# Kernel tuning notes

Measured on AMD Instinct MI355X. Metric: run time of the kernel, lower is better.

## Reference

```python
import jax, jax.numpy as jnp
import numpy as np

B, S, D_IN, D_FF, D_OUT, E = 4, 2048, 1024, 4096, 1024, 8


def setup_inputs() -> dict:
    key = jax.random.key(0)
    ks = jax.random.split(key, 8)
    s = lambda k, shape, fan: jax.random.normal(k, shape, dtype=jnp.float32) * (1.0 / np.sqrt(fan))
    return {
        "x": jax.random.normal(ks[0], (B, S, D_IN), dtype=jnp.float32),
        "switch_w": s(ks[1], (D_IN, E), D_IN),
        "switch_b": jnp.zeros((E,), dtype=jnp.float32),
        "w1": s(ks[2], (E, D_IN, D_FF), D_IN),
        "b1": jnp.zeros((E, D_FF), dtype=jnp.float32),
        "w2": s(ks[3], (E, D_FF, D_OUT), D_FF),
        "b2": jnp.zeros((E, D_OUT), dtype=jnp.float32),
    }


def reference(x, switch_w, switch_b, w1, b1, w2, b2):
    b, s, d = x.shape
    n_experts = w1.shape[0]
    xf = x.reshape(-1, d)                                   # [T, d]
    route_prob = jax.nn.softmax(xf @ switch_w + switch_b, axis=-1)  # [T, E]
    route_prob_max = jnp.max(route_prob, axis=-1)           # [T]
    routes = jnp.argmax(route_prob, axis=-1)                # [T] int, constant wrt grads

    # Per-expert FFN applied to all tokens, combined with top-1 one-hot mask
    # (drop_tokens=False -> every token goes to exactly its argmax expert).
    h = jax.nn.relu(jnp.einsum('td,edf->etf', xf, w1) + b1[:, None, :])   # [E, T, f]
    y_all = jnp.einsum('etf,efo->eto', h, w2) + b2[:, None, :]            # [E, T, d_out]
    onehot = jax.nn.one_hot(routes, n_experts, dtype=xf.dtype)            # [T, E]
    y = jnp.einsum('eto,te->to', y_all, onehot)             # dispatch-combine

    # is_scale_prob=True: scale output by routing probability
    y = y * route_prob_max[:, None]

    counts = onehot.sum(axis=0)                             # tokens per expert
    route_frac = counts / counts.sum()
    aux_loss = n_experts * jnp.sum(route_frac * route_prob.sum(axis=0))

    return y.reshape(b, s, -1), aux_loss
```

## Files before the change

kernel.cpp:

```cpp
#include <hip/hip_runtime.h>
#include <cstdint>
#include <cstddef>

#define NT   8192
#define DIN  1024
#define DFF  4096
#define DOUT 1024
#define NEXP 8

typedef float  f32x4v __attribute__((ext_vector_type(4)));
typedef short  s16x8  __attribute__((ext_vector_type(8)));
typedef short  s16x4  __attribute__((ext_vector_type(4)));

__device__ __forceinline__ ushort f2bf(float f) {
  union { float f; uint32_t u; } c; c.f = f;
  uint32_t u = c.u;
  return (ushort)((u + 0x7fffu + ((u >> 16) & 1u)) >> 16);
}

__global__ __launch_bounds__(256) void router_kernel(
    const float* __restrict__ x, const float* __restrict__ sw,
    const float* __restrict__ sb,
    int* __restrict__ routes, int* __restrict__ posArr,
    float* __restrict__ pmaxArr,
    int* __restrict__ cnt, float* __restrict__ probsum) {
  __shared__ int   sRoute[64];
  __shared__ float sProb[4][NEXP];
  __shared__ int   sBase[NEXP];

  const int lane = threadIdx.x & 63;
  const int w    = threadIdx.x >> 6;
  const int t0   = blockIdx.x * 64;

  float bias[NEXP];
#pragma unroll
  for (int e = 0; e < NEXP; e++) bias[e] = sb[e];

  float wprob[NEXP];
#pragma unroll
  for (int e = 0; e < NEXP; e++) wprob[e] = 0.0f;

  for (int k = 0; k < 16; k++) {
    const int t = t0 + w * 16 + k;
    const float* xr = x + (size_t)t * DIN;
    float acc[NEXP];
#pragma unroll
    for (int e = 0; e < NEXP; e++) acc[e] = 0.0f;
#pragma unroll
    for (int it = 0; it < DIN / 64; it++) {
      const int i = it * 64 + lane;
      const float xv = xr[i];
      const float4 s0 = *(const float4*)(sw + (size_t)i * NEXP);
      const float4 s1 = *(const float4*)(sw + (size_t)i * NEXP + 4);
      acc[0] += xv * s0.x; acc[1] += xv * s0.y; acc[2] += xv * s0.z; acc[3] += xv * s0.w;
      acc[4] += xv * s1.x; acc[5] += xv * s1.y; acc[6] += xv * s1.z; acc[7] += xv * s1.w;
    }
#pragma unroll
    for (int e = 0; e < NEXP; e++) {
#pragma unroll
      for (int off = 32; off > 0; off >>= 1) acc[e] += __shfl_xor(acc[e], off, 64);
    }
    float m = acc[0] + bias[0]; int am = 0;
    float lg[NEXP];
#pragma unroll
    for (int e = 0; e < NEXP; e++) {
      lg[e] = acc[e] + bias[e];
      if (lg[e] > m) { m = lg[e]; am = e; }
    }
    float esum = 0.0f;
    float pe[NEXP];
#pragma unroll
    for (int e = 0; e < NEXP; e++) { pe[e] = __expf(lg[e] - m); esum += pe[e]; }
    const float inv = 1.0f / esum;
#pragma unroll
    for (int e = 0; e < NEXP; e++) wprob[e] += pe[e] * inv;
    if (lane == 0) {
      routes[t] = am;
      pmaxArr[t] = inv;
      sRoute[w * 16 + k] = am;
    }
  }
  if (lane == 0) {
#pragma unroll
    for (int e = 0; e < NEXP; e++) sProb[w][e] = wprob[e];
  }
  __syncthreads();

  const int tid = threadIdx.x;
  if (tid < NEXP) {
    float s = sProb[0][tid] + sProb[1][tid] + sProb[2][tid] + sProb[3][tid];
    atomicAdd(&probsum[tid], s);
    int c = 0;
#pragma unroll
    for (int j = 0; j < 64; j++) c += (sRoute[j] == tid);
    sBase[tid] = atomicAdd(&cnt[tid], c);
  }
  __syncthreads();

  if (tid < 64) {
    const int r = sRoute[tid];
    int rank = 0;
    for (int j = 0; j < 64; j++) rank += (j < tid) & (sRoute[j] == r);
    posArr[t0 + tid] = sBase[r] + rank;
  }
}

__global__ void offsets_aux_kernel(const int* __restrict__ cnt, const float* __restrict__ probsum,
                                   int* __restrict__ offsets, float* __restrict__ auxout) {
  if (threadIdx.x == 0) {
    int o = 0; float aux = 0.0f;
    for (int e = 0; e < NEXP; e++) {
      offsets[e] = o; o += cnt[e];
      aux += (float)cnt[e] * probsum[e];
    }
    offsets[NEXP] = o;
    auxout[0] = aux * ((float)NEXP / (float)NT);
  }
}

__global__ void gather_kernel(const float* __restrict__ x, const int* __restrict__ routes,
                              const int* __restrict__ posArr, const int* __restrict__ offsets,
                              int* __restrict__ perm, ushort* __restrict__ Xg) {
  const int lane = threadIdx.x & 63;
  const int t = (blockIdx.x * blockDim.x + threadIdx.x) >> 6;
  if (t >= NT) return;
  const int slot = offsets[routes[t]] + posArr[t];
  if (lane == 0) perm[slot] = t;
  const float* src = x + (size_t)t * DIN;
  ushort* dst = Xg + (size_t)slot * DIN;
#pragma unroll
  for (int half = 0; half < 2; half++) {
    int i = half * 512 + lane * 8;
    float4 v0 = *(const float4*)(src + i);
    float4 v1 = *(const float4*)(src + i + 4);
    s16x8 p;
    p[0] = (short)f2bf(v0.x); p[1] = (short)f2bf(v0.y);
    p[2] = (short)f2bf(v0.z); p[3] = (short)f2bf(v0.w);
    p[4] = (short)f2bf(v1.x); p[5] = (short)f2bf(v1.y);
    p[6] = (short)f2bf(v1.z); p[7] = (short)f2bf(v1.w);
    *(s16x8*)(dst + i) = p;
  }
}

__global__ void transpose_cvt_kernel(const float* __restrict__ src, ushort* __restrict__ dst,
                                     const int K, const int N) {
  __shared__ float tile[64][65];
  const int ntn = N >> 6;
  const int ntk = K >> 6;
  int b = blockIdx.x;
  const int tn = b % ntn; b /= ntn;
  const int tk = b % ntk; const int e = b / ntk;
  const float* s = src + ((size_t)e * K + (size_t)tk * 64) * N + (size_t)tn * 64;
  const int c4 = (threadIdx.x & 15) * 4;
  const int r0 = threadIdx.x >> 4;
#pragma unroll
  for (int p = 0; p < 4; p++) {
    const int row = r0 + p * 16;
    float4 v = *(const float4*)(s + (size_t)row * N + c4);
    tile[row][c4 + 0] = v.x; tile[row][c4 + 1] = v.y;
    tile[row][c4 + 2] = v.z; tile[row][c4 + 3] = v.w;
  }
  __syncthreads();
  ushort* d = dst + ((size_t)e * N + (size_t)tn * 64) * K + (size_t)tk * 64;
#pragma unroll
  for (int p = 0; p < 4; p++) {
    const int nrow = r0 + p * 16;
    s16x4 o;
    o[0] = (short)f2bf(tile[c4 + 0][nrow]);
    o[1] = (short)f2bf(tile[c4 + 1][nrow]);
    o[2] = (short)f2bf(tile[c4 + 2][nrow]);
    o[3] = (short)f2bf(tile[c4 + 3][nrow]);
    *(s16x4*)(d + (size_t)nrow * K + c4) = o;
  }
}

#define GLD16(g, l)                                                                        \
  __builtin_amdgcn_global_load_lds((const __attribute__((address_space(1))) uint32_t*)(g), \
                                   (__attribute__((address_space(3))) uint32_t*)(l), 16, 0, 0)

#define SBAR()   asm volatile("s_barrier" ::: "memory")
#define WAITV(n) asm volatile("s_waitcnt vmcnt(" #n ")" ::: "memory")

template <int KDIM, int EPI>
__global__ __launch_bounds__(512, 1) void moe_gemm256_kernel(
    const ushort* __restrict__ A,
    const ushort* __restrict__ BT,
    const float* __restrict__ bias,
    const int* __restrict__ offsets,
    ushort* __restrict__ Hout,
    float* __restrict__ Y,
    const int* __restrict__ perm, const float* __restrict__ pmaxArr,
    const int N) {
  __shared__ ushort sA[4][8192];
  __shared__ ushort sB[4][8192];
  const int e = blockIdx.z;
  const int mlimit = offsets[e + 1];
  const int m0 = offsets[e] + blockIdx.y * 256;
  if (m0 >= mlimit) return;
  const int n0 = blockIdx.x * 256;
  const int tid = threadIdx.x;
  const int lane = tid & 63;
  const int wid = tid >> 6;
  const int wr = wid >> 2;
  const int wc = wid & 3;
  const int rsel = lane & 15;
  const int lhi = lane >> 4;

  const int srow = wid * 8 + (lane >> 3);
  const int scol = ((lane & 7) ^ (lane >> 3)) * 8;
  const ushort* gA = A + (size_t)(m0 + srow) * KDIM + scol;
  const ushort* gB = BT + ((size_t)e * N + n0 + srow) * KDIM + scol;
  const int ldst = tid * 8;

#define STAGE_A(s, h, kt)                                                   \
  do {                                                                      \
    const ushort* g_ = gA + (size_t)((h) * 128) * KDIM + (size_t)(kt) * 64; \
    GLD16(g_, &sA[s][ldst]);                                                \
    GLD16(g_ + (size_t)64 * KDIM, &sA[s][ldst + 4096]);                     \
  } while (0)
#define STAGE_B(s, h, kt)                                                   \
  do {                                                                      \
    const ushort* g_ = gB + (size_t)((h) * 128) * KDIM + (size_t)(kt) * 64; \
    GLD16(g_, &sB[s][ldst]);                                                \
    GLD16(g_ + (size_t)64 * KDIM, &sB[s][ldst + 4096]);                     \
  } while (0)

  f32x4v acc[2][2][4][2];
#pragma unroll
  for (int i = 0; i < 2; i++)
#pragma unroll
    for (int j = 0; j < 2; j++)
#pragma unroll
      for (int mf = 0; mf < 4; mf++)
#pragma unroll
        for (int nf = 0; nf < 2; nf++) acc[i][j][mf][nf] = (f32x4v)0.0f;

  const int rsw = rsel & 7;
  const int sw0 = ((lhi) ^ rsw) * 8;
  const int sw1 = ((4 + lhi) ^ rsw) * 8;
  int arow[4], brow[2];
#pragma unroll
  for (int mf = 0; mf < 4; mf++) arow[mf] = (wr * 64 + mf * 16 + rsel) * 64;
#pragma unroll
  for (int nf = 0; nf < 2; nf++) brow[nf] = (wc * 32 + nf * 16 + rsel) * 64;

  s16x8 a[4][2], b0[2][2], b1[2][2];

#define LDA(slot)                                                      \
  do {                                                                 \
    _Pragma("unroll") for (int mf = 0; mf < 4; mf++) {                 \
      a[mf][0] = *(const s16x8*)&sA[slot][arow[mf] + sw0];             \
      a[mf][1] = *(const s16x8*)&sA[slot][arow[mf] + sw1];             \
    }                                                                  \
  } while (0)
#define LDB(dst, slot)                                                 \
  do {                                                                 \
    _Pragma("unroll") for (int nf = 0; nf < 2; nf++) {                 \
      dst[nf][0] = *(const s16x8*)&sB[slot][brow[nf] + sw0];           \
      dst[nf][1] = *(const s16x8*)&sB[slot][brow[nf] + sw1];           \
    }                                                                  \
  } while (0)
#define MFMAQ(MG, NG, BB)                                              \
  do {                                                                 \
    __builtin_amdgcn_s_setprio(1);                                     \
    _Pragma("unroll") for (int mf = 0; mf < 4; mf++)                   \
    _Pragma("unroll") for (int nf = 0; nf < 2; nf++)                   \
    _Pragma("unroll") for (int ks = 0; ks < 2; ks++)                   \
      acc[MG][NG][mf][nf] = __builtin_amdgcn_mfma_f32_16x16x32_bf16(   \
          a[mf][ks], BB[nf][ks], acc[MG][NG][mf][nf], 0, 0, 0);        \
    __builtin_amdgcn_s_setprio(0);                                     \
  } while (0)

  constexpr int NS = KDIM / 64;
  STAGE_A(0, 0, 0);
  STAGE_B(0, 0, 0);
  STAGE_B(1, 1, 0);
  STAGE_A(1, 1, 0);
  WAITV(4);
  SBAR();

#pragma unroll 2
  for (int t = 0; t < NS; ++t) {
    const int s0 = (2 * t) & 3, s1 = (2 * t + 1) & 3;
    const int sn0 = (2 * t + 2) & 3, sn1 = (2 * t + 3) & 3;
    const bool more = (t + 1 < NS);
    LDA(s0);
    LDB(b0, s0);
    if (more) { STAGE_A(sn0, 0, t + 1); STAGE_B(sn0, 0, t + 1); }
    SBAR();
    MFMAQ(0, 0, b0);
    if (more) { WAITV(4); } else { WAITV(0); }
    SBAR();
    LDB(b1, s1);
    if (more) STAGE_B(sn1, 1, t + 1);
    SBAR();
    MFMAQ(0, 1, b1);
    SBAR();
    LDA(s1);
    if (more) STAGE_A(sn1, 1, t + 1);
    SBAR();
    MFMAQ(1, 1, b1);
    SBAR();
    MFMAQ(1, 0, b0);
    if (more) { WAITV(4); }
    SBAR();
  }
#undef LDA
#undef LDB
#undef MFMAQ
#undef STAGE_A
#undef STAGE_B

  float bv[2][2];
#pragma unroll
  for (int ng = 0; ng < 2; ng++)
#pragma unroll
    for (int nf = 0; nf < 2; nf++)
      bv[ng][nf] = bias[(size_t)e * N + n0 + ng * 128 + wc * 32 + nf * 16 + rsel];
#pragma unroll
  for (int mg = 0; mg < 2; mg++) {
#pragma unroll
    for (int mf = 0; mf < 4; mf++) {
#pragma unroll
      for (int r = 0; r < 4; r++) {
        const int grow = m0 + mg * 128 + wr * 64 + mf * 16 + lhi * 4 + r;
        if (grow < mlimit) {
          if (EPI == 0) {
            ushort* hrow = Hout + (size_t)grow * N + n0;
#pragma unroll
            for (int ng = 0; ng < 2; ng++)
#pragma unroll
              for (int nf = 0; nf < 2; nf++) {
                float v = acc[mg][ng][mf][nf][r] + bv[ng][nf];
                hrow[ng * 128 + wc * 32 + nf * 16 + rsel] = f2bf(fmaxf(v, 0.0f));
              }
          } else {
            const int tok = perm[grow];
            const float sc = pmaxArr[tok];
            float* yrow = Y + (size_t)tok * N + n0;
#pragma unroll
            for (int ng = 0; ng < 2; ng++)
#pragma unroll
              for (int nf = 0; nf < 2; nf++)
                yrow[ng * 128 + wc * 32 + nf * 16 + rsel] =
                    (acc[mg][ng][mf][nf][r] + bv[ng][nf]) * sc;
          }
        }
      }
    }
  }
}

extern "C" void kernel_launch(void* const* d_in, const int* in_sizes, int n_in,
                              void* d_out, int out_size, void* d_ws, size_t ws_size,
                              hipStream_t stream) {
  const float* x  = (const float*)d_in[0];
  const float* sw = (const float*)d_in[1];
  const float* sb = (const float*)d_in[2];
  const float* w1 = (const float*)d_in[3];
  const float* b1 = (const float*)d_in[4];
  const float* w2 = (const float*)d_in[5];
  const float* b2 = (const float*)d_in[6];
  float* out = (float*)d_out;
  float* auxp = out + (size_t)NT * DOUT;

  char* wsb = (char*)d_ws;
  int*   cnt      = (int*)wsb;
  float* probsum  = (float*)(wsb + 32);
  int*   offsets  = (int*)(wsb + 64);
  int*   routes   = (int*)(wsb + 256);
  int*   posArr   = routes + NT;
  float* pmaxArr  = (float*)(posArr + NT);
  int*   perm     = (int*)(pmaxArr + NT);
  ushort* Xg = (ushort*)(wsb + 256 + (size_t)4 * 4 * NT);
  ushort* Hg = Xg + (size_t)(NT + 256) * DIN;
  ushort* Wt = Hg + (size_t)(NT + 256) * DFF;
  size_t needed = (size_t)((char*)Wt - wsb) + (size_t)NEXP * DFF * DIN * 2;
  if (ws_size < needed) return;

  hipMemsetAsync(d_ws, 0, 64, stream);

  router_kernel<<<NT / 64, 256, 0, stream>>>(x, sw, sb, routes, posArr, pmaxArr, cnt, probsum);
  offsets_aux_kernel<<<1, 64, 0, stream>>>(cnt, probsum, offsets, auxp);
  gather_kernel<<<NT / 4, 256, 0, stream>>>(x, routes, posArr, offsets, perm, Xg);

  transpose_cvt_kernel<<<NEXP * (DIN / 64) * (DFF / 64), 256, 0, stream>>>(w1, Wt, DIN, DFF);
  moe_gemm256_kernel<DIN, 0><<<dim3(DFF / 256, 8, NEXP), 512, 0, stream>>>(
      Xg, Wt, b1, offsets, Hg, nullptr, nullptr, nullptr, DFF);

  transpose_cvt_kernel<<<NEXP * (DFF / 64) * (DOUT / 64), 256, 0, stream>>>(w2, Wt, DFF, DOUT);
  moe_gemm256_kernel<DFF, 1><<<dim3(DOUT / 256, 8, NEXP), 512, 0, stream>>>(
      Hg, Wt, b2, offsets, nullptr, out, perm, pmaxArr, DOUT);
}
```

Measured before the change: 356.7 us.

## Split-K the second expert GEMM and remap first GEMM grid for XCD locality

The down-projection GEMM is split into two K halves, doubling the number of blocks. The first half writes scaled output directly, the second writes bf16 partials that a new combine kernel adds into the output. The first GEMM uses a 1D grid remapped so each expert's tiles are grouped together, likely to improve L2 locality across XCDs. The split costs an extra partial write and read-modify-write pass, and the bf16 rounding of partials reduces accuracy.

```diff
diff --git a/kernel.cpp b/kernel.cpp
--- a/kernel.cpp
+++ b/kernel.cpp
@@ -16,6 +16,9 @@
   union { float f; uint32_t u; } c; c.f = f;
   uint32_t u = c.u;
   return (ushort)((u + 0x7fffu + ((u >> 16) & 1u)) >> 16);
+}
+__device__ __forceinline__ float bf2f(ushort h) {
+  union { uint32_t u; float f; } c; c.u = ((uint32_t)h) << 16; return c.f;
 }
 
 __global__ __launch_bounds__(256) void router_kernel(
@@ -189,15 +192,27 @@
     const int* __restrict__ offsets,
     ushort* __restrict__ Hout,
     float* __restrict__ Y,
+    ushort* __restrict__ P1,
     const int* __restrict__ perm, const float* __restrict__ pmaxArr,
-    const int N) {
+    const int N, const int LDK) {
   __shared__ ushort sA[4][8192];
   __shared__ ushort sB[4][8192];
-  const int e = blockIdx.z;
+  int e, bx, by, part;
+  if constexpr (EPI == 0) {
+    const int logical = ((blockIdx.x & 7) << 7) + (blockIdx.x >> 3);
+    e = logical >> 7;
+    bx = (logical & 127) >> 3;
+    by = logical & 7;
+    part = 0;
+  } else {
+    bx = blockIdx.x; by = blockIdx.y;
+    e = blockIdx.z & 7; part = blockIdx.z >> 3;
+  }
+  const size_t kofs = (size_t)part * KDIM;
   const int mlimit = offsets[e + 1];
-  const int m0 = offsets[e] + blockIdx.y * 256;
+  const int m0 = offsets[e] + by * 256;
   if (m0 >= mlimit) return;
-  const int n0 = blockIdx.x * 256;
+  const int n0 = bx * 256;
   const int tid = threadIdx.x;
   const int lane = tid & 63;
   const int wid = tid >> 6;
@@ -208,21 +223,21 @@
 
   const int srow = wid * 8 + (lane >> 3);
   const int scol = ((lane & 7) ^ (lane >> 3)) * 8;
-  const ushort* gA = A + (size_t)(m0 + srow) * KDIM + scol;
-  const ushort* gB = BT + ((size_t)e * N + n0 + srow) * KDIM + scol;
+  const ushort* gA = A + (size_t)(m0 + srow) * LDK + kofs + scol;
+  const ushort* gB = BT + ((size_t)e * N + n0 + srow) * LDK + kofs + scol;
   const int ldst = tid * 8;
 
-#define STAGE_A(s, h, kt)                                                   \
-  do {                                                                      \
-    const ushort* g_ = gA + (size_t)((h) * 128) * KDIM + (size_t)(kt) * 64; \
-    GLD16(g_, &sA[s][ldst]);                                                \
-    GLD16(g_ + (size_t)64 * KDIM, &sA[s][ldst + 4096]);                     \
+#define STAGE_A(s, h, kt)                                                  \
+  do {                                                                     \
+    const ushort* g_ = gA + (size_t)((h) * 128) * LDK + (size_t)(kt) * 64; \
+    GLD16(g_, &sA[s][ldst]);                                               \
+    GLD16(g_ + (size_t)64 * LDK, &sA[s][ldst + 4096]);                     \
   } while (0)
-#define STAGE_B(s, h, kt)                                                   \
-  do {                                                                      \
-    const ushort* g_ = gB + (size_t)((h) * 128) * KDIM + (size_t)(kt) * 64; \
-    GLD16(g_, &sB[s][ldst]);                                                \
-    GLD16(g_ + (size_t)64 * KDIM, &sB[s][ldst + 4096]);                     \
+#define STAGE_B(s, h, kt)                                                  \
+  do {                                                                     \
+    const ushort* g_ = gB + (size_t)((h) * 128) * LDK + (size_t)(kt) * 64; \
+    GLD16(g_, &sB[s][ldst]);                                               \
+    GLD16(g_ + (size_t)64 * LDK, &sB[s][ldst + 4096]);                     \
   } while (0)
 
   f32x4v acc[2][2][4][2];
@@ -325,7 +340,7 @@
       for (int r = 0; r < 4; r++) {
         const int grow = m0 + mg * 128 + wr * 64 + mf * 16 + lhi * 4 + r;
         if (grow < mlimit) {
-          if (EPI == 0) {
+          if constexpr (EPI == 0) {
             ushort* hrow = Hout + (size_t)grow * N + n0;
 #pragma unroll
             for (int ng = 0; ng < 2; ng++)
@@ -335,19 +350,54 @@
                 hrow[ng * 128 + wc * 32 + nf * 16 + rsel] = f2bf(fmaxf(v, 0.0f));
               }
           } else {
-            const int tok = perm[grow];
-            const float sc = pmaxArr[tok];
-            float* yrow = Y + (size_t)tok * N + n0;
-#pragma unroll
-            for (int ng = 0; ng < 2; ng++)
-#pragma unroll
-              for (int nf = 0; nf < 2; nf++)
-                yrow[ng * 128 + wc * 32 + nf * 16 + rsel] =
-                    (acc[mg][ng][mf][nf][r] + bv[ng][nf]) * sc;
+            if (part == 0) {
+              const int tok = perm[grow];
+              const float sc = pmaxArr[tok];
+              float* yrow = Y + (size_t)tok * N + n0;
+#pragma unroll
+              for (int ng = 0; ng < 2; ng++)
+#pragma unroll
+                for (int nf = 0; nf < 2; nf++)
+                  yrow[ng * 128 + wc * 32 + nf * 16 + rsel] =
+                      (acc[mg][ng][mf][nf][r] + bv[ng][nf]) * sc;
+            } else {
+              ushort* prow = P1 + (size_t)grow * N + n0;
+#pragma unroll
+              for (int ng = 0; ng < 2; ng++)
+#pragma unroll
+                for (int nf = 0; nf < 2; nf++)
+                  prow[ng * 128 + wc * 32 + nf * 16 + rsel] =
+                      f2bf(acc[mg][ng][mf][nf][r]);
+            }
           }
         }
       }
     }
+  }
+}
+
+__global__ __launch_bounds__(256) void combine_kernel(
+    const ushort* __restrict__ P1, const int* __restrict__ perm,
+    const float* __restrict__ pmaxArr, float* __restrict__ out) {
+  const int lane = threadIdx.x & 63;
+  const int slot = (blockIdx.x * blockDim.x + threadIdx.x) >> 6;
+  if (slot >= NT) return;
+  const int tok = perm[slot];
+  const float sc = pmaxArr[tok];
+  const ushort* src = P1 + (size_t)slot * DOUT;
+  float* dst = out + (size_t)tok * DOUT;
+#pragma unroll
+  for (int half = 0; half < 2; half++) {
+    const int i = half * 512 + lane * 8;
+    const s16x8 p = *(const s16x8*)(src + i);
+    float4 o0 = *(const float4*)(dst + i);
+    float4 o1 = *(const float4*)(dst + i + 4);
+    o0.x += sc * bf2f((ushort)p[0]); o0.y += sc * bf2f((ushort)p[1]);
+    o0.z += sc * bf2f((ushort)p[2]); o0.w += sc * bf2f((ushort)p[3]);
+    o1.x += sc * bf2f((ushort)p[4]); o1.y += sc * bf2f((ushort)p[5]);
+    o1.z += sc * bf2f((ushort)p[6]); o1.w += sc * bf2f((ushort)p[7]);
+    *(float4*)(dst + i) = o0;
+    *(float4*)(dst + i + 4) = o1;
   }
 }
 
@@ -377,6 +427,7 @@
   ushort* Wt = Hg + (size_t)(NT + 256) * DFF;
   size_t needed = (size_t)((char*)Wt - wsb) + (size_t)NEXP * DFF * DIN * 2;
   if (ws_size < needed) return;
+  ushort* P1 = Xg;
 
   hipMemsetAsync(d_ws, 0, 64, stream);
 
@@ -385,10 +436,11 @@
   gather_kernel<<<NT / 4, 256, 0, stream>>>(x, routes, posArr, offsets, perm, Xg);
 
   transpose_cvt_kernel<<<NEXP * (DIN / 64) * (DFF / 64), 256, 0, stream>>>(w1, Wt, DIN, DFF);
-  moe_gemm256_kernel<DIN, 0><<<dim3(DFF / 256, 8, NEXP), 512, 0, stream>>>(
-      Xg, Wt, b1, offsets, Hg, nullptr, nullptr, nullptr, DFF);
+  moe_gemm256_kernel<DIN, 0><<<1024, 512, 0, stream>>>(
+      Xg, Wt, b1, offsets, Hg, nullptr, nullptr, nullptr, nullptr, DFF, DIN);
 
   transpose_cvt_kernel<<<NEXP * (DFF / 64) * (DOUT / 64), 256, 0, stream>>>(w2, Wt, DFF, DOUT);
-  moe_gemm256_kernel<DFF, 1><<<dim3(DOUT / 256, 8, NEXP), 512, 0, stream>>>(
-      Hg, Wt, b2, offsets, nullptr, out, perm, pmaxArr, DOUT);
-}
+  moe_gemm256_kernel<DFF / 2, 3><<<dim3(DOUT / 256, 10, 16), 512, 0, stream>>>(
+      Hg, Wt, b2, offsets, nullptr, out, P1, perm, pmaxArr, DOUT, DFF);
+  combine_kernel<<<NT / 4, 256, 0, stream>>>(P1, perm, pmaxArr, out);
+}
```

Measured after the change: 393.8 us. 1.1x slower.

## Restructure MoE GEMM into 8-phase pipeline with two-tile-ahead prefetch and XCD-aware remap

Applied to the files above, without the earlier changes.

The GEMM main loop now prefetches two K-steps ahead, filling all four LDS slots up front, and waits on vmcnt(8) instead of keeping one step in flight. Each wave now covers a 128x64 output sub-tile, reading its A half and B half from slots picked by wave row and column, so LDS reads and MFMA phases are reorganised. The first GEMM also moves to a 1D grid with a remap that places each expert's tiles on a single XCD for L2 locality. The aim is better overlap of global loads with MFMA work and better cache reuse, at the cost of more loads in flight and a more complex slot scheme that is easy to get wrong.

```diff
diff --git a/kernel.cpp b/kernel.cpp
--- a/kernel.cpp
+++ b/kernel.cpp
@@ -182,7 +182,7 @@
 #define WAITV(n) asm volatile("s_waitcnt vmcnt(" #n ")" ::: "memory")
 
 template <int KDIM, int EPI>
-__global__ __launch_bounds__(512, 1) void moe_gemm256_kernel(
+__global__ __launch_bounds__(512, 1) void moe_gemm8p_kernel(
     const ushort* __restrict__ A,
     const ushort* __restrict__ BT,
     const float* __restrict__ bias,
@@ -191,18 +191,27 @@
     float* __restrict__ Y,
     const int* __restrict__ perm, const float* __restrict__ pmaxArr,
     const int N) {
-  __shared__ ushort sA[4][8192];
-  __shared__ ushort sB[4][8192];
-  const int e = blockIdx.z;
+  __shared__ ushort sA4[4][8192];
+  __shared__ ushort sB4[4][8192];
+  int e, bx, by;
+  if constexpr (EPI == 0) {
+    const int logical = ((blockIdx.x & 7) << 7) + (blockIdx.x >> 3);
+    e = logical >> 7;
+    bx = (logical & 127) >> 3;
+    by = logical & 7;
+  } else {
+    bx = blockIdx.x; by = blockIdx.y; e = blockIdx.z;
+  }
   const int mlimit = offsets[e + 1];
-  const int m0 = offsets[e] + blockIdx.y * 256;
+  const int m0 = offsets[e] + by * 256;
   if (m0 >= mlimit) return;
-  const int n0 = blockIdx.x * 256;
+  const int n0 = bx * 256;
   const int tid = threadIdx.x;
   const int lane = tid & 63;
   const int wid = tid >> 6;
   const int wr = wid >> 2;
   const int wc = wid & 3;
+  const int hb = wc >> 1;
   const int rsel = lane & 15;
   const int lhi = lane >> 4;
 
@@ -211,139 +220,134 @@
   const ushort* gA = A + (size_t)(m0 + srow) * KDIM + scol;
   const ushort* gB = BT + ((size_t)e * N + n0 + srow) * KDIM + scol;
   const int ldst = tid * 8;
-
-#define STAGE_A(s, h, kt)                                                   \
-  do {                                                                      \
-    const ushort* g_ = gA + (size_t)((h) * 128) * KDIM + (size_t)(kt) * 64; \
-    GLD16(g_, &sA[s][ldst]);                                                \
-    GLD16(g_ + (size_t)64 * KDIM, &sA[s][ldst + 4096]);                     \
-  } while (0)
-#define STAGE_B(s, h, kt)                                                   \
-  do {                                                                      \
-    const ushort* g_ = gB + (size_t)((h) * 128) * KDIM + (size_t)(kt) * 64; \
-    GLD16(g_, &sB[s][ldst]);                                                \
-    GLD16(g_ + (size_t)64 * KDIM, &sB[s][ldst + 4096]);                     \
-  } while (0)
-
-  f32x4v acc[2][2][4][2];
-#pragma unroll
-  for (int i = 0; i < 2; i++)
-#pragma unroll
-    for (int j = 0; j < 2; j++)
-#pragma unroll
-      for (int mf = 0; mf < 4; mf++)
-#pragma unroll
-        for (int nf = 0; nf < 2; nf++) acc[i][j][mf][nf] = (f32x4v)0.0f;
+  const size_t LK = (size_t)KDIM;
+
+#define STAGE_A(s, h, kt)                                              \
+  do {                                                                 \
+    const ushort* g_ = gA + (size_t)((h) * 128) * LK + (size_t)(kt) * 64; \
+    GLD16(g_, &sA4[s][ldst]);                                          \
+    GLD16(g_ + 64 * LK, &sA4[s][ldst + 4096]);                         \
+  } while (0)
+#define STAGE_B(s, h, kt)                                              \
+  do {                                                                 \
+    const ushort* g_ = gB + (size_t)((h) * 128) * LK + (size_t)(kt) * 64; \
+    GLD16(g_, &sB4[s][ldst]);                                          \
+    GLD16(g_ + 64 * LK, &sB4[s][ldst + 4096]);                         \
+  } while (0)
+
+  f32x4v acc[2][4][4];
+#pragma unroll
+  for (int g = 0; g < 2; g++)
+#pragma unroll
+    for (int mf = 0; mf < 4; mf++)
+#pragma unroll
+      for (int nf = 0; nf < 4; nf++) acc[g][mf][nf] = (f32x4v)0.0f;
 
   const int rsw = rsel & 7;
   const int sw0 = ((lhi) ^ rsw) * 8;
   const int sw1 = ((4 + lhi) ^ rsw) * 8;
-  int arow[4], brow[2];
-#pragma unroll
-  for (int mf = 0; mf < 4; mf++) arow[mf] = (wr * 64 + mf * 16 + rsel) * 64;
-#pragma unroll
-  for (int nf = 0; nf < 2; nf++) brow[nf] = (wc * 32 + nf * 16 + rsel) * 64;
+  const int arow0 = rsel * 64;
+  const int brow0 = ((wc & 1) * 64 + rsel) * 64;
 
   s16x8 a[4][2], b0[2][2], b1[2][2];
 
-#define LDA(slot)                                                      \
+#define LDA03(slot)                                                    \
   do {                                                                 \
     _Pragma("unroll") for (int mf = 0; mf < 4; mf++) {                 \
-      a[mf][0] = *(const s16x8*)&sA[slot][arow[mf] + sw0];             \
-      a[mf][1] = *(const s16x8*)&sA[slot][arow[mf] + sw1];             \
+      a[mf][0] = *(const s16x8*)&sA4[slot][arow0 + mf * 1024 + sw0];   \
+      a[mf][1] = *(const s16x8*)&sA4[slot][arow0 + mf * 1024 + sw1];   \
     }                                                                  \
   } while (0)
-#define LDB(dst, slot)                                                 \
+#define LDA47(slot)                                                    \
+  do {                                                                 \
+    _Pragma("unroll") for (int mf = 0; mf < 4; mf++) {                 \
+      a[mf][0] = *(const s16x8*)&sA4[slot][arow0 + 4096 + mf * 1024 + sw0]; \
+      a[mf][1] = *(const s16x8*)&sA4[slot][arow0 + 4096 + mf * 1024 + sw1]; \
+    }                                                                  \
+  } while (0)
+#define LDB2(dst, slot, nfb)                                           \
   do {                                                                 \
     _Pragma("unroll") for (int nf = 0; nf < 2; nf++) {                 \
-      dst[nf][0] = *(const s16x8*)&sB[slot][brow[nf] + sw0];           \
-      dst[nf][1] = *(const s16x8*)&sB[slot][brow[nf] + sw1];           \
+      dst[nf][0] = *(const s16x8*)&sB4[slot][brow0 + ((nfb) + nf) * 1024 + sw0]; \
+      dst[nf][1] = *(const s16x8*)&sB4[slot][brow0 + ((nfb) + nf) * 1024 + sw1]; \
     }                                                                  \
   } while (0)
-#define MFMAQ(MG, NG, BB)                                              \
+#define MFMAPH(MG, BB, NFB)                                            \
   do {                                                                 \
     __builtin_amdgcn_s_setprio(1);                                     \
     _Pragma("unroll") for (int mf = 0; mf < 4; mf++)                   \
     _Pragma("unroll") for (int nf = 0; nf < 2; nf++)                   \
     _Pragma("unroll") for (int ks = 0; ks < 2; ks++)                   \
-      acc[MG][NG][mf][nf] = __builtin_amdgcn_mfma_f32_16x16x32_bf16(   \
-          a[mf][ks], BB[nf][ks], acc[MG][NG][mf][nf], 0, 0, 0);        \
+      acc[MG][mf][(NFB) + nf] = __builtin_amdgcn_mfma_f32_16x16x32_bf16( \
+          a[mf][ks], BB[nf][ks], acc[MG][mf][(NFB) + nf], 0, 0, 0);    \
     __builtin_amdgcn_s_setprio(0);                                     \
   } while (0)
 
   constexpr int NS = KDIM / 64;
-  STAGE_A(0, 0, 0);
-  STAGE_B(0, 0, 0);
-  STAGE_B(1, 1, 0);
-  STAGE_A(1, 1, 0);
-  WAITV(4);
+  STAGE_A(0, 0, 0); STAGE_A(1, 1, 0); STAGE_B(0, 0, 0); STAGE_B(1, 1, 0);
+  STAGE_B(2, 0, 1); STAGE_B(3, 1, 1); STAGE_A(2, 0, 1); STAGE_A(3, 1, 1);
+  WAITV(8);
   SBAR();
 
 #pragma unroll 2
   for (int t = 0; t < NS; ++t) {
-    const int s0 = (2 * t) & 3, s1 = (2 * t + 1) & 3;
-    const int sn0 = (2 * t + 2) & 3, sn1 = (2 * t + 3) & 3;
-    const bool more = (t + 1 < NS);
-    LDA(s0);
-    LDB(b0, s0);
-    if (more) { STAGE_A(sn0, 0, t + 1); STAGE_B(sn0, 0, t + 1); }
-    SBAR();
-    MFMAQ(0, 0, b0);
-    if (more) { WAITV(4); } else { WAITV(0); }
-    SBAR();
-    LDB(b1, s1);
-    if (more) STAGE_B(sn1, 1, t + 1);
-    SBAR();
-    MFMAQ(0, 1, b1);
-    SBAR();
-    LDA(s1);
-    if (more) STAGE_A(sn1, 1, t + 1);
-    SBAR();
-    MFMAQ(1, 1, b1);
-    SBAR();
-    MFMAQ(1, 0, b0);
-    if (more) { WAITV(4); }
-    SBAR();
-  }
-#undef LDA
-#undef LDB
-#undef MFMAQ
+    const int sa = (2 * t + wr) & 3;
+    const int sb = (2 * t + hb) & 3;
+    const int r0s = (2 * t) & 3, r1s = (2 * t + 1) & 3;
+    const bool st2 = (t + 2 < NS);
+    LDA03(sa);
+    LDB2(b0, sb, 0);
+    SBAR();
+    MFMAPH(0, b0, 0);
+    SBAR();
+    LDB2(b1, sb, 2);
+    SBAR();
+    MFMAPH(0, b1, 2);
+    SBAR();
+    LDA47(sa);
+    if (st2) { STAGE_B(r0s, 0, t + 2); STAGE_B(r1s, 1, t + 2); }
+    SBAR();
+    MFMAPH(1, b1, 2);
+    SBAR();
+    if (st2) { STAGE_A(r0s, 0, t + 2); STAGE_A(r1s, 1, t + 2); }
+    SBAR();
+    MFMAPH(1, b0, 0);
+    if (st2) { WAITV(8); } else { WAITV(0); }
+    SBAR();
+  }
+#undef LDA03
+#undef LDA47
+#undef LDB2
+#undef MFMAPH
 #undef STAGE_A
 #undef STAGE_B
 
-  float bv[2][2];
-#pragma unroll
-  for (int ng = 0; ng < 2; ng++)
-#pragma unroll
-    for (int nf = 0; nf < 2; nf++)
-      bv[ng][nf] = bias[(size_t)e * N + n0 + ng * 128 + wc * 32 + nf * 16 + rsel];
+  float bv[4];
+#pragma unroll
+  for (int nf = 0; nf < 4; nf++)
+    bv[nf] = bias[(size_t)e * N + n0 + wc * 64 + nf * 16 + rsel];
 #pragma unroll
   for (int mg = 0; mg < 2; mg++) {
 #pragma unroll
     for (int mf = 0; mf < 4; mf++) {
 #pragma unroll
       for (int r = 0; r < 4; r++) {
-        const int grow = m0 + mg * 128 + wr * 64 + mf * 16 + lhi * 4 + r;
+        const int grow = m0 + wr * 128 + mg * 64 + mf * 16 + lhi * 4 + r;
         if (grow < mlimit) {
-          if (EPI == 0) {
-            ushort* hrow = Hout + (size_t)grow * N + n0;
-#pragma unroll
-            for (int ng = 0; ng < 2; ng++)
-#pragma unroll
-              for (int nf = 0; nf < 2; nf++) {
-                float v = acc[mg][ng][mf][nf][r] + bv[ng][nf];
-                hrow[ng * 128 + wc * 32 + nf * 16 + rsel] = f2bf(fmaxf(v, 0.0f));
-              }
+          if constexpr (EPI == 0) {
+            ushort* hrow = Hout + (size_t)grow * N + n0 + wc * 64;
+#pragma unroll
+            for (int nf = 0; nf < 4; nf++) {
+              float v = acc[mg][mf][nf][r] + bv[nf];
+              hrow[nf * 16 + rsel] = f2bf(fmaxf(v, 0.0f));
+            }
           } else {
             const int tok = perm[grow];
             const float sc = pmaxArr[tok];
-            float* yrow = Y + (size_t)tok * N + n0;
-#pragma unroll
-            for (int ng = 0; ng < 2; ng++)
-#pragma unroll
-              for (int nf = 0; nf < 2; nf++)
-                yrow[ng * 128 + wc * 32 + nf * 16 + rsel] =
-                    (acc[mg][ng][mf][nf][r] + bv[ng][nf]) * sc;
+            float* yrow = Y + (size_t)tok * N + n0 + wc * 64;
+#pragma unroll
+            for (int nf = 0; nf < 4; nf++)
+              yrow[nf * 16 + rsel] = (acc[mg][mf][nf][r] + bv[nf]) * sc;
           }
         }
       }
@@ -385,10 +389,10 @@
   gather_kernel<<<NT / 4, 256, 0, stream>>>(x, routes, posArr, offsets, perm, Xg);
 
   transpose_cvt_kernel<<<NEXP * (DIN / 64) * (DFF / 64), 256, 0, stream>>>(w1, Wt, DIN, DFF);
-  moe_gemm256_kernel<DIN, 0><<<dim3(DFF / 256, 8, NEXP), 512, 0, stream>>>(
+  moe_gemm8p_kernel<DIN, 0><<<1024, 512, 0, stream>>>(
       Xg, Wt, b1, offsets, Hg, nullptr, nullptr, nullptr, DFF);
 
   transpose_cvt_kernel<<<NEXP * (DFF / 64) * (DOUT / 64), 256, 0, stream>>>(w2, Wt, DFF, DOUT);
-  moe_gemm256_kernel<DFF, 1><<<dim3(DOUT / 256, 8, NEXP), 512, 0, stream>>>(
+  moe_gemm8p_kernel<DFF, 1><<<dim3(DOUT / 256, 8, NEXP), 512, 0, stream>>>(
       Hg, Wt, b2, offsets, nullptr, out, perm, pmaxArr, DOUT);
 }
```

Result: slower. 393.4 us (+10.3%).
